# Kernel optimization log

Measured on AMD Instinct MI355X. Metric: run time of the kernel, lower is better.

Reference implementation:

```python
import jax, jax.numpy as jnp
import numpy as np

B = 8
M = 500_000
XSIZE = 128


def setup_inputs() -> dict:
    key = jax.random.key(0)
    k1, k2 = jax.random.split(key)
    indices = jax.random.randint(k1, (B, M, 3), 0, XSIZE, dtype=jnp.int32)
    values = jax.random.normal(k2, (B, M), dtype=jnp.float32)
    return {"indices": indices, "values": values, "xsize": XSIZE}


def reference(indices, values, xsize):
    # Batched scatter-add density accumulation (tensor_scatter_nd_add per sample)
    def scatter_one(idx, val):
        grid = jnp.zeros((xsize, xsize, xsize), dtype=val.dtype)
        return grid.at[idx[:, 0], idx[:, 1], idx[:, 2]].add(val)

    grid = jax.vmap(scatter_one)(indices, values)  # (B, X, X, X)

    # Adjacent voxel differences along each spatial axis
    d1 = grid[:, 1:, :, :] - grid[:, :-1, :, :]
    d2 = grid[:, :, 1:, :] - grid[:, :, :-1, :]
    d3 = grid[:, :, :, 1:] - grid[:, :, :, :-1]

    ax = (1, 2, 3)
    # Total variation loss: normalized by total voxel count xsize^3
    num_pixels = jnp.float32(xsize * xsize * xsize)
    tv = (jnp.sum(jnp.abs(d1), axis=ax)
          + jnp.sum(jnp.abs(d2), axis=ax)
          + jnp.sum(jnp.abs(d3), axis=ax)) / num_pixels

    # MSE smoothness loss: normalizer matches TF code (2*X*X - X - X)
    num_pairs = jnp.float32(2 * xsize * xsize - 2 * xsize)
    mse = (jnp.sum(jnp.square(d1), axis=ax)
           + jnp.sum(jnp.square(d2), axis=ax)
           + jnp.sum(jnp.square(d3), axis=ax)) / num_pairs

    return jnp.stack([tv, mse])  # (2, B)
```

## Files before the change

### kernel.cpp

```cpp
#include <hip/hip_runtime.h>
#include <stdint.h>

#define BATCH 8
#define MPTS 500000
#define NPTS (BATCH * MPTS)
#define NBQ 1024
#define TP 8192
#define NTILE ((NPTS + TP - 1) / TP)
#define HROW (NBQ + 1)
#define NIFACE 304
#define NBND (BATCH * NIFACE)

template <int NT>
__device__ __forceinline__ void block_reduce2(float& tv, float& mse) {
    for (int off = 32; off > 0; off >>= 1) {
        tv  += __shfl_down(tv, off, 64);
        mse += __shfl_down(mse, off, 64);
    }
    __shared__ float stv[NT / 64], sms[NT / 64];
    int w = threadIdx.x >> 6, lane = threadIdx.x & 63;
    if (lane == 0) { stv[w] = tv; sms[w] = mse; }
    __syncthreads();
    if (threadIdx.x == 0) {
        float a = 0.f, m = 0.f;
        #pragma unroll
        for (int e = 0; e < NT / 64; ++e) { a += stv[e]; m += sms[e]; }
        tv = a; mse = m;
    }
}

__device__ __forceinline__ uint32_t pack_aux(int b, int i, int j, int k) {
    uint32_t q = ((uint32_t)b << 7) | ((uint32_t)(i >> 5) << 5) |
                 ((uint32_t)(j >> 5) << 3) | (uint32_t)(k >> 4);
    uint32_t l = ((uint32_t)(i & 31) << 9) | ((uint32_t)(j & 31) << 4) | (uint32_t)(k & 15);
    return (q << 14) | l;
}

__device__ __forceinline__ int gaddr(int s, int kl) {
    return s * 16 + (kl & 3) + ((((kl >> 2) ^ (s >> 1)) & 3) << 2);
}
__device__ __forceinline__ int goff(int s, int c) {
    return ((c ^ (s >> 1)) & 3) << 2;
}

__device__ __forceinline__ uint32_t val16(float f) {
    return (__float_as_uint(f) + 0x8000u) >> 16;
}

__global__ void __launch_bounds__(1024, 8) sort_k(const int* __restrict__ idx,
                                                  const float* __restrict__ val,
                                                  uint16_t* __restrict__ hoff,
                                                  uint32_t* __restrict__ rec) {
    __shared__ uint32_t h[NBQ];
    __shared__ uint32_t wtot[16];
    __shared__ uint32_t srt[TP];
    int tile = blockIdx.x;
    int p0 = tile * TP;
    int cnt = min(TP, NPTS - p0);
    h[threadIdx.x] = 0;
    __syncthreads();
    uint32_t a[8]; uint32_t vpk[4];
    int ng = cnt >> 2;
    #pragma unroll
    for (int e = 0; e < 2; ++e) {
        int g = threadIdx.x + e * 1024;
        if (g < ng) {
            int p = p0 + g * 4;
            const int4* ip = (const int4*)(idx + (size_t)p * 3);
            int4 A = ip[0], B = ip[1], C = ip[2];
            float4 V = *(const float4*)(val + p);
            int b = p / MPTS;
            a[4*e+0] = pack_aux(b, A.x, A.y, A.z);
            a[4*e+1] = pack_aux(b, A.w, B.x, B.y);
            a[4*e+2] = pack_aux(b, B.z, B.w, C.x);
            a[4*e+3] = pack_aux(b, C.y, C.z, C.w);
            vpk[2*e]     = val16(V.x) | (val16(V.y) << 16);
            vpk[2*e + 1] = val16(V.z) | (val16(V.w) << 16);
            #pragma unroll
            for (int u = 0; u < 4; ++u) atomicAdd(&h[a[4*e+u] >> 14], 1u);
        } else {
            a[4*e+0] = a[4*e+1] = a[4*e+2] = a[4*e+3] = 0xFFFFFFFFu;
            vpk[2*e] = vpk[2*e + 1] = 0u;
        }
    }
    __syncthreads();
    int q = threadIdx.x, lane = q & 63, wave = q >> 6;
    uint32_t cq = h[q];
    uint32_t inc = cq;
    #pragma unroll
    for (int off = 1; off < 64; off <<= 1) {
        uint32_t n = __shfl_up(inc, off, 64);
        if (lane >= off) inc += n;
    }
    if (lane == 63) wtot[wave] = inc;
    __syncthreads();
    if (q < 16) {
        uint32_t w = wtot[q];
        #pragma unroll
        for (int off = 1; off < 16; off <<= 1) {
            uint32_t n = __shfl_up(w, off, 16);
            if (q >= off) w += n;
        }
        wtot[q] = w;
    }
    __syncthreads();
    uint32_t lstart = (wave ? wtot[wave - 1] : 0u) + inc - cq;
    hoff[(size_t)tile * HROW + q] = (uint16_t)lstart;
    if (q == 0) hoff[(size_t)tile * HROW + NBQ] = (uint16_t)cnt;
    h[q] = lstart;
    __syncthreads();
    #pragma unroll
    for (int e = 0; e < 8; ++e) {
        if (a[e] != 0xFFFFFFFFu) {
            uint32_t qq = a[e] >> 14;
            uint32_t u = (vpk[e >> 1] >> ((e & 1) * 16)) & 0xFFFFu;
            srt[atomicAdd(&h[qq], 1u)] = (u << 16) | (a[e] & 16383u);
        }
    }
    __syncthreads();
    uint4* recq = (uint4*)(rec + (size_t)tile * TP);
    const uint4* sr4 = (const uint4*)srt;
    for (int s = threadIdx.x; s < (cnt >> 2); s += 1024) recq[s] = sr4[s];
}

__global__ void __launch_bounds__(1024, 8) accum_k(const uint32_t* __restrict__ rec,
                                                   const uint16_t* __restrict__ hoff,
                                                   uint16_t* __restrict__ faces,
                                                   float2* __restrict__ pa) {
    __shared__ float g[16384];
    __shared__ uint16_t sA[NTILE], sB[NTILE];
    int qb = ((blockIdx.x & 7) << 7) | (blockIdx.x >> 3);
    if (threadIdx.x < NTILE) {
        const uint16_t* row = hoff + (size_t)threadIdx.x * HROW + qb;
        sA[threadIdx.x] = row[0];
        sB[threadIdx.x] = row[1];
    }
    {
        float4 z = make_float4(0.f, 0.f, 0.f, 0.f);
        #pragma unroll
        for (int c = 0; c < 4; ++c)
            *(float4*)&g[(threadIdx.x + c * 1024) * 4] = z;
    }
    __syncthreads();
    {
        int grp = threadIdx.x >> 3;
        int r8  = threadIdx.x & 7;
        for (int t = grp; t < NTILE; t += 128) {
            uint32_t a0 = sA[t], a1 = sB[t];
            const uint32_t* rp = rec + (size_t)t * TP;
            for (uint32_t r = a0 + r8; r < a1; r += 8) {
                uint32_t e = rp[r];
                int l = e & 16383;
                atomicAdd(&g[gaddr(l >> 4, l & 15)], __uint_as_float(e & 0xFFFF0000u));
            }
        }
    }
    __syncthreads();
    float tv = 0.f, mse = 0.f;
    {
        int s = threadIdx.x;
        int jl = s & 31, il = s >> 5;
        bool jin = jl < 31, iin = il < 31;
        float own[16];
        #pragma unroll
        for (int c = 0; c < 4; ++c)
            *(float4*)&own[c * 4] = *(const float4*)&g[s * 16 + goff(s, c)];
        #pragma unroll
        for (int k = 0; k < 15; ++k) {
            float d = own[k + 1] - own[k]; tv += fabsf(d); mse += d * d;
        }
        #pragma unroll
        for (int hh = 0; hh < 2; ++hh) {
            if (jin) {
                float jn[8];
                *(float4*)&jn[0] = *(const float4*)&g[(s + 1) * 16 + goff(s + 1, 2 * hh)];
                *(float4*)&jn[4] = *(const float4*)&g[(s + 1) * 16 + goff(s + 1, 2 * hh + 1)];
                #pragma unroll
                for (int k = 0; k < 8; ++k) {
                    float d = jn[k] - own[8 * hh + k]; tv += fabsf(d); mse += d * d;
                }
            }
            if (iin) {
                float inb[8];
                *(float4*)&inb[0] = *(const float4*)&g[(s + 32) * 16 + goff(s + 32, 2 * hh)];
                *(float4*)&inb[4] = *(const float4*)&g[(s + 32) * 16 + goff(s + 32, 2 * hh + 1)];
                #pragma unroll
                for (int k = 0; k < 8; ++k) {
                    float d = inb[k] - own[8 * hh + k]; tv += fabsf(d); mse += d * d;
                }
            }
        }
    }
    {
        uint16_t* f = faces + (size_t)qb * 4096;
        int t = threadIdx.x;
        if (t < 512) {
            int hi = t >> 4, lo = t & 15;
            f[t]        = (uint16_t)(__float_as_uint(g[gaddr(hi, lo)]) >> 16);
            f[512 + t]  = (uint16_t)(__float_as_uint(g[gaddr(992 + hi, lo)]) >> 16);
            f[1024 + t] = (uint16_t)(__float_as_uint(g[gaddr(hi * 32, lo)]) >> 16);
            f[1536 + t] = (uint16_t)(__float_as_uint(g[gaddr(hi * 32 + 31, lo)]) >> 16);
        }
        f[2048 + t] = (uint16_t)(__float_as_uint(g[gaddr(t, 0)]) >> 16);
        f[3072 + t] = (uint16_t)(__float_as_uint(g[gaddr(t, 15)]) >> 16);
    }
    block_reduce2<1024>(tv, mse);
    if (threadIdx.x == 0) pa[qb] = make_float2(tv, mse);
}

__device__ __forceinline__ float f16up(uint16_t u) {
    return __uint_as_float(((uint32_t)u) << 16);
}

__global__ void __launch_bounds__(256) boundary_k(const uint16_t* __restrict__ faces,
                                                  float2* __restrict__ pb) {
    int x = blockIdx.x;
    int b = x / NIFACE;
    int r = x - b * NIFACE;
    int qA, qB, fA, fB, elems;
    if (r < 96) {
        int s = r >> 5, u = (r >> 3) & 3, w = r & 7;
        qA = (b << 7) | (s << 5) | (u << 3) | w; qB = qA + 32;
        fA = 512; fB = 0; elems = 512;
    } else if (r < 192) {
        int r2 = r - 96;
        int s = r2 >> 5, u = (r2 >> 3) & 3, w = r2 & 7;
        qA = (b << 7) | (u << 5) | (s << 3) | w; qB = qA + 8;
        fA = 1536; fB = 1024; elems = 512;
    } else {
        int r2 = r - 192;
        int s = r2 >> 4, u = (r2 >> 2) & 3, v = r2 & 3;
        qA = (b << 7) | (u << 5) | (v << 3) | s; qB = qA + 1;
        fA = 3072; fB = 2048; elems = 1024;
    }
    const uint16_t* pA = faces + (size_t)qA * 4096 + fA;
    const uint16_t* pB = faces + (size_t)qB * 4096 + fB;
    float tv = 0.f, mse = 0.f;
    for (int e = threadIdx.x; e < elems; e += 256) {
        float d = f16up(pB[e]) - f16up(pA[e]);
        tv += fabsf(d); mse += d * d;
    }
    block_reduce2<256>(tv, mse);
    if (threadIdx.x == 0) pb[x] = make_float2(tv, mse);
}

__global__ void __launch_bounds__(256) final_k(const float2* __restrict__ pa,
                                               const float2* __restrict__ pb,
                                               float* __restrict__ out) {
    int b = blockIdx.x;
    float tv = 0.f, mse = 0.f;
    const float2* a = pa + (size_t)b * (NBQ / BATCH);
    for (int i = threadIdx.x; i < NBQ / BATCH; i += 256) { float2 v = a[i]; tv += v.x; mse += v.y; }
    const float2* p = pb + (size_t)b * NIFACE;
    for (int i = threadIdx.x; i < NIFACE; i += 256) { float2 v = p[i]; tv += v.x; mse += v.y; }
    block_reduce2<256>(tv, mse);
    if (threadIdx.x == 0) {
        out[b]     = tv  * (1.f / 2097152.f);
        out[8 + b] = mse * (1.f / 32512.f);
    }
}

extern "C" void kernel_launch(void* const* d_in, const int* in_sizes, int n_in,
                              void* d_out, int out_size, void* d_ws, size_t ws_size,
                              hipStream_t stream) {
    const int*   indices = (const int*)d_in[0];
    const float* values  = (const float*)d_in[1];
    float*       out     = (float*)d_out;

    char* wp = (char*)d_ws;
    uint16_t* hoff  = (uint16_t*)wp;
    wp += (((size_t)NTILE * HROW * 2) + 255) & ~(size_t)255;
    float2*   pa    = (float2*)wp;
    wp += (NBQ * 8 + 255) & ~(size_t)255;
    float2*   pb    = (float2*)wp;
    wp += ((size_t)NBND * 8 + 255) & ~(size_t)255;
    uint32_t* rec   = (uint32_t*)wp;
    wp += (((size_t)NTILE * TP * 4) + 255) & ~(size_t)255;
    uint16_t* faces = (uint16_t*)wp;

    sort_k    <<<NTILE, 1024, 0, stream>>>(indices, values, hoff, rec);
    accum_k   <<<NBQ,   1024, 0, stream>>>(rec, hoff, faces, pa);
    boundary_k<<<NBND,  256,  0, stream>>>(faces, pb);
    final_k   <<<BATCH, 256,  0, stream>>>(pa, pb, out);
}
```

Measured before the change: 135.7 us.

## Fuse boundary and final reduction into accum kernel via last-block counter

Removes the separate boundary-face and final reduction kernels. Each accum block atomically increments a per-batch counter, and the last block for a batch sums that batch's partials and computes all cross-brick face differences itself before writing the output. This is meant to eliminate two kernel launches and their inter-kernel gaps. The cost is that the boundary work for each batch is now serialized onto a single block at the tail of the kernel instead of being spread across thousands of blocks.

```diff
diff --git a/kernel.cpp b/kernel.cpp
--- a/kernel.cpp
+++ b/kernel.cpp
@@ -8,8 +8,9 @@
 #define TP 8192
 #define NTILE ((NPTS + TP - 1) / TP)
 #define HROW (NBQ + 1)
-#define NIFACE 304
-#define NBND (BATCH * NIFACE)
+#define FEL1 49152
+#define FEL2 98304
+#define FELT 212992
 
 template <int NT>
 __device__ __forceinline__ void block_reduce2(float& tv, float& mse) {
@@ -46,15 +47,20 @@
 __device__ __forceinline__ uint32_t val16(float f) {
     return (__float_as_uint(f) + 0x8000u) >> 16;
 }
+__device__ __forceinline__ float f16up(uint16_t u) {
+    return __uint_as_float(((uint32_t)u) << 16);
+}
 
 __global__ void __launch_bounds__(1024, 8) sort_k(const int* __restrict__ idx,
                                                   const float* __restrict__ val,
                                                   uint16_t* __restrict__ hoff,
-                                                  uint32_t* __restrict__ rec) {
+                                                  uint32_t* __restrict__ rec,
+                                                  uint32_t* __restrict__ cnt8) {
     __shared__ uint32_t h[NBQ];
     __shared__ uint32_t wtot[16];
     __shared__ uint32_t srt[TP];
     int tile = blockIdx.x;
+    if (tile == 0 && threadIdx.x < BATCH) cnt8[threadIdx.x] = 0u;
     int p0 = tile * TP;
     int cnt = min(TP, NPTS - p0);
     h[threadIdx.x] = 0;
@@ -126,10 +132,14 @@
 __global__ void __launch_bounds__(1024, 8) accum_k(const uint32_t* __restrict__ rec,
                                                    const uint16_t* __restrict__ hoff,
                                                    uint16_t* __restrict__ faces,
-                                                   float2* __restrict__ pa) {
+                                                   float2* __restrict__ pa,
+                                                   uint32_t* __restrict__ cnt8,
+                                                   float* __restrict__ out) {
     __shared__ float g[16384];
     __shared__ uint16_t sA[NTILE], sB[NTILE];
+    __shared__ uint32_t slast;
     int qb = ((blockIdx.x & 7) << 7) | (blockIdx.x >> 3);
+    int b = qb >> 7;
     if (threadIdx.x < NTILE) {
         const uint16_t* row = hoff + (size_t)threadIdx.x * HROW + qb;
         sA[threadIdx.x] = row[0];
@@ -206,57 +216,45 @@
     }
     block_reduce2<1024>(tv, mse);
     if (threadIdx.x == 0) pa[qb] = make_float2(tv, mse);
-}
-
-__device__ __forceinline__ float f16up(uint16_t u) {
-    return __uint_as_float(((uint32_t)u) << 16);
-}
-
-__global__ void __launch_bounds__(256) boundary_k(const uint16_t* __restrict__ faces,
-                                                  float2* __restrict__ pb) {
-    int x = blockIdx.x;
-    int b = x / NIFACE;
-    int r = x - b * NIFACE;
-    int qA, qB, fA, fB, elems;
-    if (r < 96) {
-        int s = r >> 5, u = (r >> 3) & 3, w = r & 7;
-        qA = (b << 7) | (s << 5) | (u << 3) | w; qB = qA + 32;
-        fA = 512; fB = 0; elems = 512;
-    } else if (r < 192) {
-        int r2 = r - 96;
-        int s = r2 >> 5, u = (r2 >> 3) & 3, w = r2 & 7;
-        qA = (b << 7) | (u << 5) | (s << 3) | w; qB = qA + 8;
-        fA = 1536; fB = 1024; elems = 512;
-    } else {
-        int r2 = r - 192;
-        int s = r2 >> 4, u = (r2 >> 2) & 3, v = r2 & 3;
-        qA = (b << 7) | (u << 5) | (v << 3) | s; qB = qA + 1;
-        fA = 3072; fB = 2048; elems = 1024;
-    }
-    const uint16_t* pA = faces + (size_t)qA * 4096 + fA;
-    const uint16_t* pB = faces + (size_t)qB * 4096 + fB;
-    float tv = 0.f, mse = 0.f;
-    for (int e = threadIdx.x; e < elems; e += 256) {
-        float d = f16up(pB[e]) - f16up(pA[e]);
-        tv += fabsf(d); mse += d * d;
-    }
-    block_reduce2<256>(tv, mse);
-    if (threadIdx.x == 0) pb[x] = make_float2(tv, mse);
-}
-
-__global__ void __launch_bounds__(256) final_k(const float2* __restrict__ pa,
-                                               const float2* __restrict__ pb,
-                                               float* __restrict__ out) {
-    int b = blockIdx.x;
-    float tv = 0.f, mse = 0.f;
-    const float2* a = pa + (size_t)b * (NBQ / BATCH);
-    for (int i = threadIdx.x; i < NBQ / BATCH; i += 256) { float2 v = a[i]; tv += v.x; mse += v.y; }
-    const float2* p = pb + (size_t)b * NIFACE;
-    for (int i = threadIdx.x; i < NIFACE; i += 256) { float2 v = p[i]; tv += v.x; mse += v.y; }
-    block_reduce2<256>(tv, mse);
-    if (threadIdx.x == 0) {
-        out[b]     = tv  * (1.f / 2097152.f);
-        out[8 + b] = mse * (1.f / 32512.f);
+    __threadfence();
+    __syncthreads();
+    if (threadIdx.x == 0) slast = atomicAdd(&cnt8[b], 1u);
+    __syncthreads();
+    if (slast == 127u) {
+        __threadfence();
+        float tv2 = 0.f, mse2 = 0.f;
+        for (int i = threadIdx.x; i < NBQ / BATCH; i += 1024) {
+            float2 v = pa[b * (NBQ / BATCH) + i]; tv2 += v.x; mse2 += v.y;
+        }
+        for (int f = threadIdx.x; f < FELT; f += 1024) {
+            int qA, qB, fA, fB, e;
+            if (f < FEL1) {
+                int r = f >> 9; e = f & 511;
+                int s = r >> 5, u = (r >> 3) & 3, w = r & 7;
+                qA = (b << 7) | (s << 5) | (u << 3) | w; qB = qA + 32;
+                fA = 512; fB = 0;
+            } else if (f < FEL2) {
+                int f2 = f - FEL1;
+                int r = f2 >> 9; e = f2 & 511;
+                int s = r >> 5, u = (r >> 3) & 3, w = r & 7;
+                qA = (b << 7) | (u << 5) | (s << 3) | w; qB = qA + 8;
+                fA = 1536; fB = 1024;
+            } else {
+                int f2 = f - FEL2;
+                int r = f2 >> 10; e = f2 & 1023;
+                int s = r >> 4, u = (r >> 2) & 3, v = r & 3;
+                qA = (b << 7) | (u << 5) | (v << 3) | s; qB = qA + 1;
+                fA = 3072; fB = 2048;
+            }
+            float d = f16up(faces[(size_t)qB * 4096 + fB + e]) -
+                      f16up(faces[(size_t)qA * 4096 + fA + e]);
+            tv2 += fabsf(d); mse2 += d * d;
+        }
+        block_reduce2<1024>(tv2, mse2);
+        if (threadIdx.x == 0) {
+            out[b]     = tv2  * (1.f / 2097152.f);
+            out[8 + b] = mse2 * (1.f / 32512.f);
+        }
     }
 }
 
@@ -272,14 +270,12 @@
     wp += (((size_t)NTILE * HROW * 2) + 255) & ~(size_t)255;
     float2*   pa    = (float2*)wp;
     wp += (NBQ * 8 + 255) & ~(size_t)255;
-    float2*   pb    = (float2*)wp;
-    wp += ((size_t)NBND * 8 + 255) & ~(size_t)255;
+    uint32_t* cnt8  = (uint32_t*)wp;
+    wp += (BATCH * 4 + 255) & ~(size_t)255;
     uint32_t* rec   = (uint32_t*)wp;
     wp += (((size_t)NTILE * TP * 4) + 255) & ~(size_t)255;
     uint16_t* faces = (uint16_t*)wp;
 
-    sort_k    <<<NTILE, 1024, 0, stream>>>(indices, values, hoff, rec);
-    accum_k   <<<NBQ,   1024, 0, stream>>>(rec, hoff, faces, pa);
-    boundary_k<<<NBND,  256,  0, stream>>>(faces, pb);
-    final_k   <<<BATCH, 256,  0, stream>>>(pa, pb, out);
-}
+    sort_k <<<NTILE, 1024, 0, stream>>>(indices, values, hoff, rec, cnt8);
+    accum_k<<<NBQ,   1024, 0, stream>>>(rec, hoff, faces, pa, cnt8, out);
+}
```

New measurement: 476.3 us. 251% more time.
